# Kernel optimization log

Measured on AMD Instinct MI355X. Metric: run time of the kernel, lower is better.

The kernel has to match this reference:

```python
import jax, jax.numpy as jnp
import numpy as np

D = 768
H = 12
DK = D // H
FF = 3072
EPS = 1e-5


def layernorm(x, g, b):
    mu = jnp.mean(x, axis=-1, keepdims=True)
    var = jnp.mean((x - mu) ** 2, axis=-1, keepdims=True)
    return (x - mu) * jax.lax.rsqrt(var + EPS) * g + b


def setup_inputs() -> dict:
    key = jax.random.key(0)
    ks = jax.random.split(key, 12)
    B, S = 4, 2048
    s = 0.02
    return {
        "embedding": jax.random.normal(ks[0], (B, S, D), jnp.float32),
        "mask": jnp.ones((B, 1, 1, S), jnp.int32),
        "Wq": jax.random.normal(ks[1], (D, D), jnp.float32) * s,
        "bq": jnp.zeros((D,), jnp.float32),
        "Wk": jax.random.normal(ks[2], (D, D), jnp.float32) * s,
        "bk": jnp.zeros((D,), jnp.float32),
        "Wv": jax.random.normal(ks[3], (D, D), jnp.float32) * s,
        "bv": jnp.zeros((D,), jnp.float32),
        "Wo": jax.random.normal(ks[4], (D, D), jnp.float32) * s,
        "bo": jnp.zeros((D,), jnp.float32),
        "W1": jax.random.normal(ks[5], (D, FF), jnp.float32) * s,
        "b1": jnp.zeros((FF,), jnp.float32),
        "W2": jax.random.normal(ks[6], (FF, D), jnp.float32) * s,
        "b2": jnp.zeros((D,), jnp.float32),
        "ln_g": jnp.ones((D,), jnp.float32),
        "ln_b": jnp.zeros((D,), jnp.float32),
    }


def reference(embedding, mask, Wq, bq, Wk, bk, Wv, bv, Wo, bo, W1, b1, W2, b2, ln_g, ln_b):
    B, S, _ = embedding.shape
    # QKV projections -> [B, H, S, DK]
    def split_heads(t):
        return t.reshape(B, S, H, DK).transpose(0, 2, 1, 3)
    q = split_heads(embedding @ Wq + bq)
    k = split_heads(embedding @ Wk + bk)
    v = split_heads(embedding @ Wv + bv)
    scores = jnp.einsum("bhqd,bhkd->bhqk", q, k) / jnp.sqrt(jnp.float32(DK))
    scores = jnp.where(mask == 0, jnp.float32(-1e9), scores)
    weights = jax.nn.softmax(scores, axis=-1)  # dropout = identity (eval)
    context = jnp.einsum("bhqk,bhkd->bhqd", weights, v)
    context = context.transpose(0, 2, 1, 3).reshape(B, S, D)
    attn_out = context @ Wo + bo
    x = layernorm(attn_out + embedding, ln_g, ln_b)
    ff = jax.nn.relu(x @ W1 + b1) @ W2 + b2
    return layernorm(x + ff, ln_g, ln_b)
```

## Files before the change

kernel.cpp:

```cpp
#include <hip/hip_runtime.h>

#define D_MODEL 768
#define NHEADS  12
#define SEQ     2048
#define BATCH   4
#define FF_DIM  3072
#define NTOK    (BATCH * SEQ)

typedef short short8 __attribute__((ext_vector_type(8)));
typedef float f32x4 __attribute__((ext_vector_type(4)));
typedef float f32x16 __attribute__((ext_vector_type(16)));
typedef int int4v __attribute__((ext_vector_type(4)));
typedef int int2v __attribute__((ext_vector_type(2)));
typedef unsigned short ushort4v __attribute__((ext_vector_type(4)));
typedef float float4v __attribute__((ext_vector_type(4)));

__device__ __forceinline__ short f2bf(float x) {
  unsigned u = __builtin_bit_cast(unsigned, x);
  u += 0x7fffu + ((u >> 16) & 1u);
  return (short)(u >> 16);
}
__device__ __forceinline__ float bf2f(short x) {
  return __builtin_bit_cast(float, ((unsigned)(unsigned short)x) << 16);
}
__device__ __forceinline__ int cvtpk(float a, float b) {
  int r;
  asm("v_cvt_pk_bf16_f32 %0, %1, %2" : "=v"(r) : "v"(a), "v"(b));
  return r;
}
__device__ __forceinline__ float fexp2(float x) {
#if __has_builtin(__builtin_amdgcn_exp2f)
  return __builtin_amdgcn_exp2f(x);
#else
  return exp2f(x);
#endif
}
__device__ __forceinline__ float frcp(float x) {
#if __has_builtin(__builtin_amdgcn_rcpf)
  return __builtin_amdgcn_rcpf(x);
#else
  return 1.f / x;
#endif
}
__device__ __forceinline__ void gll16(const void* g, void* l) {
  __builtin_amdgcn_global_load_lds(
      (const __attribute__((address_space(1))) void*)g,
      (__attribute__((address_space(3))) void*)l, 16, 0, 0);
}

__device__ __forceinline__ void wt_tile(float (*T)[65], const float* __restrict__ W,
                                        short* __restrict__ Wt, int K, int N,
                                        int bx, int by, int t) {
  const int c = t & 63, rb = t >> 6;
  const int k0 = by * 64, n0 = bx * 64;
#pragma unroll
  for (int i = 0; i < 16; ++i) {
    const int r = rb * 16 + i;
    T[c][r] = W[(size_t)(k0 + r) * N + n0 + c];
  }
  __syncthreads();
#pragma unroll
  for (int j = 0; j < 16; ++j) {
    const int idx = t + j * 256;
    const int nl = idx >> 6, kl = idx & 63;
    Wt[(size_t)(n0 + nl) * K + k0 + kl] = f2bf(T[nl][kl]);
  }
}

__global__ __launch_bounds__(256) void prep(
    const float* __restrict__ Wq, const float* __restrict__ Wk, const float* __restrict__ Wv,
    const float* __restrict__ Wo, const float* __restrict__ W1, const float* __restrict__ W2,
    const float* __restrict__ bq, const float* __restrict__ bk, const float* __restrict__ bv,
    const float* __restrict__ emb,
    short* __restrict__ wqkvt, short* __restrict__ wot, short* __restrict__ w1t,
    short* __restrict__ w2t, float* __restrict__ bqkv, short* __restrict__ x0) {
  __shared__ float T[64][65];
  const int bi = blockIdx.x;
  const int t = threadIdx.x;
  if (bi < 432) {
    const int s = bi / 144, l = bi % 144;
    const float* W = (s == 0) ? Wq : (s == 1) ? Wk : Wv;
    wt_tile(T, W, wqkvt + (size_t)s * 768 * 768, 768, 768, l % 12, l / 12, t);
  } else if (bi < 576) {
    const int l = bi - 432;
    wt_tile(T, Wo, wot, 768, 768, l % 12, l / 12, t);
  } else if (bi < 1152) {
    const int l = bi - 576;
    wt_tile(T, W1, w1t, 768, 3072, l % 48, l / 48, t);
  } else if (bi < 1728) {
    const int l = bi - 1152;
    wt_tile(T, W2, w2t, 3072, 768, l % 12, l / 12, t);
  } else if (bi == 1728) {
#pragma unroll
    for (int j = 0; j < 9; ++j) {
      const int i = t + j * 256;
      bqkv[i] = (i < 768) ? bq[i] : (i < 1536) ? bk[i - 768] : bv[i - 1536];
    }
  } else {
    const int i = (bi - 1729) * 256 + t;
    float4v v = *(const float4v*)(emb + (size_t)i * 4);
    ushort4v p;
    p[0] = (unsigned short)f2bf(v[0]);
    p[1] = (unsigned short)f2bf(v[1]);
    p[2] = (unsigned short)f2bf(v[2]);
    p[3] = (unsigned short)f2bf(v[3]);
    *(ushort4v*)(x0 + (size_t)i * 4) = p;
  }
}

enum { EPI_QKV = 0, EPI_WO = 1, EPI_RELU = 2, EPI_FF = 3 };

template <int EPI>
__global__ __launch_bounds__(256) void gemm_bt(const short* __restrict__ A,
                                               const short* __restrict__ Bt,
                                               const float* __restrict__ bias,
                                               const float* __restrict__ extraF,
                                               const short* __restrict__ extraB,
                                               void* __restrict__ outp,
                                               int M, int N, int K) {
  __shared__ short As[128 * 64];
  __shared__ short Bs[128 * 64];
  const int tid = threadIdx.x;
  const int lane = tid & 63, wid = tid >> 6;
  const int wr = wid >> 1, wc = wid & 1;
  const int l16 = lane & 15, lg = lane >> 4;
  const int brow = blockIdx.y * 128, bcol = blockIdx.x * 128;

  f32x4 acc[4][4];
#pragma unroll
  for (int i = 0; i < 4; ++i)
#pragma unroll
    for (int j = 0; j < 4; ++j) acc[i][j] = (f32x4){0.f, 0.f, 0.f, 0.f};

  for (int kt = 0; kt < K; kt += 64) {
    __syncthreads();
#pragma unroll
    for (int i = 0; i < 4; ++i) {
      const int c = wid * 256 + i * 64 + lane;
      const int row = c >> 3;
      const int gc = (c & 7) ^ (row & 7);
      gll16(A + (size_t)(brow + row) * K + kt + gc * 8,
            (char*)As + (wid * 256 + i * 64) * 16);
      gll16(Bt + (size_t)(bcol + row) * K + kt + gc * 8,
            (char*)Bs + (wid * 256 + i * 64) * 16);
    }
    __syncthreads();
#pragma unroll
    for (int kc = 0; kc < 2; ++kc) {
      short8 af[4], bfr[4];
#pragma unroll
      for (int m = 0; m < 4; ++m) {
        const int row = wr * 64 + m * 16 + l16;
        const int ch = (kc * 4 + lg) ^ (row & 7);
        af[m] = *(const short8*)((const char*)As + row * 128 + ch * 16);
      }
#pragma unroll
      for (int n = 0; n < 4; ++n) {
        const int row = wc * 64 + n * 16 + l16;
        const int ch = (kc * 4 + lg) ^ (row & 7);
        bfr[n] = *(const short8*)((const char*)Bs + row * 128 + ch * 16);
      }
#pragma unroll
      for (int m = 0; m < 4; ++m)
#pragma unroll
        for (int n = 0; n < 4; ++n)
          acc[m][n] = __builtin_amdgcn_mfma_f32_16x16x32_bf16(af[m], bfr[n],
                                                              acc[m][n], 0, 0, 0);
    }
  }

  const int mbase = brow + wr * 64;
  const int nbase = bcol + wc * 64;

  if constexpr (EPI == EPI_QKV) {
    short* qb_ = (short*)outp;
    short* kb_ = qb_ + (size_t)NTOK * D_MODEL;
    short* vt_ = kb_ + (size_t)NTOK * D_MODEL;
    const int type = nbase / 768;
#pragma unroll
    for (int ni = 0; ni < 4; ++ni) {
      const int n = nbase + ni * 16 + l16;
      const float bv = bias[n];
      const int ncol = n - type * 768;
      const int h = ncol >> 6, dk = ncol & 63;
      if (type == 2) {
#pragma unroll
        for (int mi = 0; mi < 4; ++mi) {
          const int m0 = mbase + mi * 16 + lg * 4;
          const int bidx = m0 >> 11, s0 = m0 & 2047;
          ushort4v pk;
#pragma unroll
          for (int r = 0; r < 4; ++r) pk[r] = (unsigned short)f2bf(acc[mi][ni][r] + bv);
          *(ushort4v*)(vt_ + (((size_t)bidx * NHEADS + h) * 64 + dk) * SEQ + s0) = pk;
        }
      } else {
        short* o = (type == 0) ? qb_ : kb_;
        const float sc = (type == 0) ? 0.125f * 1.44269504f : 1.f;
#pragma unroll
        for (int mi = 0; mi < 4; ++mi) {
#pragma unroll
          for (int r = 0; r < 4; ++r) {
            const int m = mbase + mi * 16 + lg * 4 + r;
            const int bidx = m >> 11, sidx = m & 2047;
            o[(((size_t)bidx * NHEADS + h) * SEQ + sidx) * 64 + dk] =
                f2bf((acc[mi][ni][r] + bv) * sc);
          }
        }
      }
    }
  } else if constexpr (EPI == EPI_WO) {
    short* o = (short*)outp;
#pragma unroll
    for (int ni = 0; ni < 4; ++ni) {
      const int n = nbase + ni * 16 + l16;
      const float bv = bias[n];
#pragma unroll
      for (int mi = 0; mi < 4; ++mi)
#pragma unroll
        for (int r = 0; r < 4; ++r) {
          const int m = mbase + mi * 16 + lg * 4 + r;
          const size_t idx = (size_t)m * N + n;
          o[idx] = f2bf(acc[mi][ni][r] + bv + extraF[idx]);
        }
    }
  } else if constexpr (EPI == EPI_FF) {
    short* o = (short*)outp;
#pragma unroll
    for (int ni = 0; ni < 4; ++ni) {
      const int n = nbase + ni * 16 + l16;
      const float bv = bias[n];
#pragma unroll
      for (int mi = 0; mi < 4; ++mi)
#pragma unroll
        for (int r = 0; r < 4; ++r) {
          const int m = mbase + mi * 16 + lg * 4 + r;
          const size_t idx = (size_t)m * N + n;
          o[idx] = f2bf(acc[mi][ni][r] + bv + bf2f(extraB[idx]));
        }
    }
  } else {
    short* o = (short*)outp;
#pragma unroll
    for (int ni = 0; ni < 4; ++ni) {
      const int n = nbase + ni * 16 + l16;
      const float bv = bias[n];
#pragma unroll
      for (int mi = 0; mi < 4; ++mi)
#pragma unroll
        for (int r = 0; r < 4; ++r) {
          const int m = mbase + mi * 16 + lg * 4 + r;
          o[(size_t)m * N + n] = f2bf(fmaxf(acc[mi][ni][r] + bv, 0.f));
        }
    }
  }
}

__global__ __launch_bounds__(256) void attn_fa6(
    const short* __restrict__ Q,
    const short* __restrict__ Kb,
    const short* __restrict__ Vt,
    const int* __restrict__ mask,
    float* __restrict__ opart,
    float* __restrict__ lpart) {
  __shared__ short KsA[64 * 64], KsB[64 * 64];
  __shared__ short VsA[64 * 64], VsB[64 * 64];
  const int tid = threadIdx.x;
  const int lane = tid & 63, w = tid >> 6;
  const int l31 = lane & 31, hi = lane >> 5;

  const int i = blockIdx.x;
  const int r8 = i & 7, qq = i >> 3;
  const int bhz = ((qq >> 3) << 3) + r8;
  const int qblk = qq & 7;
  const int half = bhz / 48, bh = bhz % 48;
  const int b = bh / NHEADS;
  const int q0 = qblk * 256 + w * 64;
  const int kvbase = half * (SEQ / 2);

  const short* qpA = Q + ((size_t)bh * SEQ + q0 + l31) * 64;
  const short* qpB = qpA + 32 * 64;
  short8 qfA[4], qfB[4];
#pragma unroll
  for (int s = 0; s < 4; ++s) {
    qfA[s] = *(const short8*)(qpA + s * 16 + hi * 8);
    qfB[s] = *(const short8*)(qpB + s * 16 + hi * 8);
  }

  f32x16 o0a, o1a, o0b, o1b;
#pragma unroll
  for (int k = 0; k < 16; ++k) { o0a[k] = 0.f; o1a[k] = 0.f; o0b[k] = 0.f; o1b[k] = 0.f; }
  float lA = 0.f, lB = 0.f;

  auto stage = [&](short* Ksd, short* Vsd, int kv0) {
#pragma unroll
    for (int i2 = 0; i2 < 2; ++i2) {
      const int c = i2 * 256 + tid;
      const int row = c >> 3;
      const int gc = (c & 7) ^ (row & 7);
      gll16(Kb + ((size_t)bh * SEQ + kv0 + row) * 64 + gc * 8,
            (char*)Ksd + (i2 * 256 + w * 64) * 16);
      gll16(Vt + ((size_t)bh * 64 + row) * SEQ + kv0 + gc * 8,
            (char*)Vsd + (i2 * 256 + w * 64) * 16);
    }
  };

  stage(KsA, VsA, kvbase);
  __syncthreads();

  for (int t = 0; t < SEQ / 2 / 64; ++t) {
    const short* Ksc = (t & 1) ? KsB : KsA;
    const short* Vsc = (t & 1) ? VsB : VsA;

    const int mv = mask[(size_t)b * SEQ + kvbase + t * 64 + lane];
    const bool anym = __any(mv == 0);
    float ra = 0.f, rb_ = 0.f;
    short8 paA[4], paB[4];

#pragma unroll
    for (int ph = 0; ph < 2; ++ph) {
      f32x16 sa, sb;
#pragma unroll
      for (int k = 0; k < 16; ++k) { sa[k] = 0.f; sb[k] = 0.f; }
      const char* kr = (const char*)Ksc + (ph * 32 + l31) * 128;
#pragma unroll
      for (int slot = 0; slot < 4; ++slot) {
        const int ch = (slot * 2 + hi) ^ (l31 & 7);
        short8 kf = *(const short8*)(kr + ch * 16);
        sa = __builtin_amdgcn_mfma_f32_32x32x16_bf16(kf, qfA[slot], sa, 0, 0, 0);
        sb = __builtin_amdgcn_mfma_f32_32x32x16_bf16(kf, qfB[slot], sb, 0, 0, 0);
      }
      if (ph == 1 && t + 1 < SEQ / 2 / 64)
        stage((t & 1) ? KsA : KsB, (t & 1) ? VsA : VsB, kvbase + (t + 1) * 64);
      if (anym) {
#pragma unroll
        for (int r = 0; r < 16; ++r) {
          const int cr = ph * 32 + (r & 3) + 8 * (r >> 2) + 4 * hi;
          if (__shfl(mv, cr) == 0) { sa[r] = -1e9f; sb[r] = -1e9f; }
        }
      }
#pragma unroll
      for (int r = 0; r < 16; ++r) {
        sa[r] = fexp2(sa[r]);
        sb[r] = fexp2(sb[r]);
        ra += sa[r];
        rb_ += sb[r];
      }
#pragma unroll
      for (int ks = 0; ks < 2; ++ks) {
        const int rb0 = ks * 8;
#pragma unroll
        for (int g = 0; g < 2; ++g) {
          const f32x16& sc = g ? sb : sa;
          int x0_ = cvtpk(sc[rb0 + 0], sc[rb0 + 1]);
          int y0_ = cvtpk(sc[rb0 + 4], sc[rb0 + 5]);
          int x1_ = cvtpk(sc[rb0 + 2], sc[rb0 + 3]);
          int y1_ = cvtpk(sc[rb0 + 6], sc[rb0 + 7]);
          int4v pw;
#if __has_builtin(__builtin_amdgcn_permlane32_swap)
          int2v r0 = __builtin_amdgcn_permlane32_swap(x0_, y0_, false, false);
          int2v r1 = __builtin_amdgcn_permlane32_swap(x1_, y1_, false, false);
          pw[0] = r0[0]; pw[1] = r1[0]; pw[2] = r0[1]; pw[3] = r1[1];
#else
          const int ys0 = __shfl_xor(y0_, 32);
          const int xs0 = __shfl_xor(x0_, 32);
          const int ys1 = __shfl_xor(y1_, 32);
          const int xs1 = __shfl_xor(x1_, 32);
          pw[0] = hi ? ys0 : x0_;
          pw[1] = hi ? ys1 : x1_;
          pw[2] = hi ? y0_ : xs0;
          pw[3] = hi ? y1_ : xs1;
#endif
          const short8 pa = __builtin_bit_cast(short8, pw);
          if (g) paB[ph * 2 + ks] = pa; else paA[ph * 2 + ks] = pa;
        }
      }
    }
    lA += ra + __shfl_xor(ra, 32);
    lB += rb_ + __shfl_xor(rb_, 32);

#pragma unroll
    for (int vs = 0; vs < 4; ++vs) {
      const int vch = (vs * 2 + hi) ^ (l31 & 7);
      short8 vb0 = *(const short8*)((const char*)Vsc + l31 * 128 + vch * 16);
      short8 vb1 = *(const short8*)((const char*)Vsc + (32 + l31) * 128 + vch * 16);
      o0a = __builtin_amdgcn_mfma_f32_32x32x16_bf16(paA[vs], vb0, o0a, 0, 0, 0);
      o0b = __builtin_amdgcn_mfma_f32_32x32x16_bf16(paB[vs], vb0, o0b, 0, 0, 0);
      o1a = __builtin_amdgcn_mfma_f32_32x32x16_bf16(paA[vs], vb1, o1a, 0, 0, 0);
      o1b = __builtin_amdgcn_mfma_f32_32x32x16_bf16(paB[vs], vb1, o1b, 0, 0, 0);
    }
    __syncthreads();
  }

  float* opA = opart + ((size_t)half * BATCH * NHEADS + bh) * SEQ * 64;
#pragma unroll
  for (int r = 0; r < 16; ++r) {
    const int q = (r & 3) + 8 * (r >> 2) + 4 * hi;
    float* pa_ = opA + (size_t)(q0 + q) * 64;
    pa_[l31] = o0a[r];
    pa_[32 + l31] = o1a[r];
    float* pb_ = opA + (size_t)(q0 + 32 + q) * 64;
    pb_[l31] = o0b[r];
    pb_[32 + l31] = o1b[r];
  }
  if (lane < 32) {
    float* lp = lpart + (size_t)half * BATCH * NHEADS * SEQ + (size_t)bh * SEQ + q0;
    lp[l31] = lA;
    lp[32 + l31] = lB;
  }
}

__global__ __launch_bounds__(256) void attn_combine(const float* __restrict__ op,
                                                    const float* __restrict__ lp,
                                                    short* __restrict__ ctx) {
  const size_t HS = (size_t)BATCH * NHEADS * SEQ * 64;
  const int i4 = blockIdx.x * 256 + threadIdx.x;
  const size_t base = (size_t)i4 * 4;
  float4v a = *(const float4v*)(op + base);
  float4v c = *(const float4v*)(op + HS + base);
  const int row = (int)(base >> 6);
  const float inv = frcp(lp[row] + lp[BATCH * NHEADS * SEQ + row]);
  const int bh = row >> 11, q = row & 2047;
  const int b = bh / NHEADS, h = bh - b * NHEADS;
  const int dk = (int)(base & 63);
  ushort4v o;
#pragma unroll
  for (int j = 0; j < 4; ++j) o[j] = (unsigned short)f2bf((a[j] + c[j]) * inv);
  *(ushort4v*)(ctx + ((size_t)b * SEQ + q) * D_MODEL + h * 64 + dk) = o;
}

template <int OUT_F32>
__global__ __launch_bounds__(256) void ln_w(const short* __restrict__ y,
                                            const float* __restrict__ gw,
                                            const float* __restrict__ bw,
                                            float* __restrict__ of,
                                            short* __restrict__ ob) {
  const int lane = threadIdx.x & 63, w = threadIdx.x >> 6;
  const int row = blockIdx.x * 4 + w;
  const short* yr = y + (size_t)row * D_MODEL;
  short8 v8 = *(const short8*)(yr + lane * 8);
  ushort4v v4 = *(const ushort4v*)(yr + 512 + lane * 4);
  float f[12];
#pragma unroll
  for (int j = 0; j < 8; ++j) f[j] = bf2f(v8[j]);
#pragma unroll
  for (int j = 0; j < 4; ++j) f[8 + j] = bf2f((short)v4[j]);
  float s = 0.f, q = 0.f;
#pragma unroll
  for (int j = 0; j < 12; ++j) { s += f[j]; q += f[j] * f[j]; }
#pragma unroll
  for (int mm = 1; mm < 64; mm <<= 1) {
    s += __shfl_xor(s, mm);
    q += __shfl_xor(q, mm);
  }
  const float mu = s * (1.f / D_MODEL);
  const float rs = rsqrtf(q * (1.f / D_MODEL) - mu * mu + 1e-5f);
  float4v g0 = *(const float4v*)(gw + lane * 8);
  float4v g1 = *(const float4v*)(gw + lane * 8 + 4);
  float4v g2 = *(const float4v*)(gw + 512 + lane * 4);
  float4v b0 = *(const float4v*)(bw + lane * 8);
  float4v b1 = *(const float4v*)(bw + lane * 8 + 4);
  float4v b2 = *(const float4v*)(bw + 512 + lane * 4);
  float o[12];
#pragma unroll
  for (int j = 0; j < 4; ++j) o[j] = (f[j] - mu) * rs * g0[j] + b0[j];
#pragma unroll
  for (int j = 0; j < 4; ++j) o[4 + j] = (f[4 + j] - mu) * rs * g1[j] + b1[j];
#pragma unroll
  for (int j = 0; j < 4; ++j) o[8 + j] = (f[8 + j] - mu) * rs * g2[j] + b2[j];
  if constexpr (OUT_F32) {
    float* orow = of + (size_t)row * D_MODEL;
    float4v t0, t1, t2;
#pragma unroll
    for (int j = 0; j < 4; ++j) { t0[j] = o[j]; t1[j] = o[4 + j]; t2[j] = o[8 + j]; }
    *(float4v*)(orow + lane * 8) = t0;
    *(float4v*)(orow + lane * 8 + 4) = t1;
    *(float4v*)(orow + 512 + lane * 4) = t2;
  } else {
    short* orow = ob + (size_t)row * D_MODEL;
    ushort4v t0, t1, t2;
#pragma unroll
    for (int j = 0; j < 4; ++j) {
      t0[j] = (unsigned short)f2bf(o[j]);
      t1[j] = (unsigned short)f2bf(o[4 + j]);
      t2[j] = (unsigned short)f2bf(o[8 + j]);
    }
    *(ushort4v*)(orow + lane * 8) = t0;
    *(ushort4v*)(orow + lane * 8 + 4) = t1;
    *(ushort4v*)(orow + 512 + lane * 4) = t2;
  }
}

extern "C" void kernel_launch(void* const* d_in, const int* in_sizes, int n_in,
                              void* d_out, int out_size, void* d_ws, size_t ws_size,
                              hipStream_t stream) {
  const float* emb = (const float*)d_in[0];
  const int* mask = (const int*)d_in[1];
  const float* Wq = (const float*)d_in[2];
  const float* bq = (const float*)d_in[3];
  const float* Wk = (const float*)d_in[4];
  const float* bk = (const float*)d_in[5];
  const float* Wv = (const float*)d_in[6];
  const float* bv = (const float*)d_in[7];
  const float* Wo = (const float*)d_in[8];
  const float* bo = (const float*)d_in[9];
  const float* W1 = (const float*)d_in[10];
  const float* b1 = (const float*)d_in[11];
  const float* W2 = (const float*)d_in[12];
  const float* b2 = (const float*)d_in[13];
  const float* lng = (const float*)d_in[14];
  const float* lnb = (const float*)d_in[15];

  char* ws = (char*)d_ws;
  size_t off = 0;
  auto alloc = [&](size_t bytes) -> char* {
    char* p = ws + off;
    off = (off + bytes + 255) & ~(size_t)255;
    return p;
  };
  const size_t DD = (size_t)D_MODEL * D_MODEL;
  const size_t DF = (size_t)D_MODEL * FF_DIM;
  const size_t TD = (size_t)NTOK * D_MODEL;
  const size_t TF = (size_t)NTOK * FF_DIM;

  short* wqkvt = (short*)alloc(3 * DD * 2);
  short* wot = (short*)alloc(DD * 2);
  short* w1t = (short*)alloc(DF * 2);
  short* w2t = (short*)alloc(DF * 2);
  float* bqkv = (float*)alloc(2304 * 4);
  short* x0 = (short*)alloc(TD * 2);
  short* qkv = (short*)alloc(3 * TD * 2);
  short* aresb = (short*)alloc(TD * 2);
  short* xbf = (short*)alloc(TD * 2);
  short* hbf = (short*)alloc(TF * 2);
  short* ffresb = (short*)alloc(TD * 2);
  float* lpart = (float*)alloc(2 * (size_t)BATCH * NHEADS * SEQ * 4);
  short* qb = qkv;
  short* kb = qkv + TD;
  short* vtb = qkv + 2 * TD;
  short* ctx = x0;
  float* opart = (float*)hbf;

  prep<<<dim3(1729 + (int)(TD / 1024)), 256, 0, stream>>>(
      Wq, Wk, Wv, Wo, W1, W2, bq, bk, bv, emb, wqkvt, wot, w1t, w2t, bqkv, x0);
  gemm_bt<EPI_QKV><<<dim3(18, 64), 256, 0, stream>>>(
      x0, wqkvt, bqkv, nullptr, nullptr, qkv, NTOK, 3 * D_MODEL, D_MODEL);
  attn_fa6<<<dim3(768), 256, 0, stream>>>(qb, kb, vtb, mask, opart, lpart);
  attn_combine<<<dim3((int)((size_t)BATCH * NHEADS * SEQ * 64 / 4 / 256)), 256, 0, stream>>>(
      opart, lpart, ctx);
  gemm_bt<EPI_WO><<<dim3(6, 64), 256, 0, stream>>>(
      ctx, wot, bo, emb, nullptr, aresb, NTOK, D_MODEL, D_MODEL);
  ln_w<0><<<dim3(NTOK / 4), 256, 0, stream>>>(aresb, lng, lnb, nullptr, xbf);
  gemm_bt<EPI_RELU><<<dim3(24, 64), 256, 0, stream>>>(
      xbf, w1t, b1, nullptr, nullptr, hbf, NTOK, FF_DIM, D_MODEL);
  gemm_bt<EPI_FF><<<dim3(6, 64), 256, 0, stream>>>(
      hbf, w2t, b2, nullptr, xbf, ffresb, NTOK, D_MODEL, FF_DIM);
  ln_w<1><<<dim3(NTOK / 4), 256, 0, stream>>>(ffresb, lng, lnb, (float*)d_out, nullptr);
}
```

Before: 299.0 us.

## Store K/V in MFMA fragment layout and stream attention operands from global

The QKV GEMM epilogue now writes K and V pre-permuted into the exact per-lane fragment order the 32x32x16 MFMA operands need. The attention kernel can then load K and V straight from global memory into registers, with no LDS staging and no per-tile __syncthreads. K tiles are double-buffered in registers, and the kernel processes 32 keys per step instead of 64. This removes LDS traffic, swizzle arithmetic and block barriers, but each of the four waves now fetches the same K/V data on its own, so more load pressure falls on the caches. The last prefetch also reads one tile past each key range.

```diff
diff --git a/kernel.cpp b/kernel.cpp
--- a/kernel.cpp
+++ b/kernel.cpp
@@ -174,8 +174,8 @@
 
   if constexpr (EPI == EPI_QKV) {
     short* qb_ = (short*)outp;
-    short* kb_ = qb_ + (size_t)NTOK * D_MODEL;
-    short* vt_ = kb_ + (size_t)NTOK * D_MODEL;
+    short* kf_ = qb_ + (size_t)NTOK * D_MODEL;
+    short* vf_ = kf_ + (size_t)NTOK * D_MODEL;
     const int type = nbase / 768;
 #pragma unroll
     for (int ni = 0; ni < 4; ++ni) {
@@ -183,28 +183,45 @@
       const float bv = bias[n];
       const int ncol = n - type * 768;
       const int h = ncol >> 6, dk = ncol & 63;
-      if (type == 2) {
+      if (type == 0) {
+#pragma unroll
+        for (int mi = 0; mi < 4; ++mi) {
+#pragma unroll
+          for (int r = 0; r < 4; ++r) {
+            const int m = mbase + mi * 16 + lg * 4 + r;
+            const int bidx = m >> 11, sidx = m & 2047;
+            qb_[(((size_t)bidx * NHEADS + h) * SEQ + sidx) * 64 + dk] =
+                f2bf((acc[mi][ni][r] + bv) * (0.125f * 1.44269504f));
+          }
+        }
+      } else if (type == 1) {
+        const int slot = dk >> 4, dhi = (dk >> 3) & 1, e = dk & 7;
+#pragma unroll
+        for (int mi = 0; mi < 4; ++mi) {
+#pragma unroll
+          for (int r = 0; r < 4; ++r) {
+            const int m = mbase + mi * 16 + lg * 4 + r;
+            const int bidx = m >> 11, sidx = m & 2047;
+            const size_t bh = (size_t)bidx * NHEADS + h;
+            const size_t idx =
+                (((bh * 64 + (sidx >> 5)) * 4 + slot) * 64 + ((sidx & 31) + dhi * 32)) * 8 + e;
+            kf_[idx] = f2bf(acc[mi][ni][r] + bv);
+          }
+        }
+      } else {
+        const int dblk = dk >> 5, lanef = dk & 31;
 #pragma unroll
         for (int mi = 0; mi < 4; ++mi) {
           const int m0 = mbase + mi * 16 + lg * 4;
           const int bidx = m0 >> 11, s0 = m0 & 2047;
+          const size_t bh = (size_t)bidx * NHEADS + h;
           ushort4v pk;
 #pragma unroll
           for (int r = 0; r < 4; ++r) pk[r] = (unsigned short)f2bf(acc[mi][ni][r] + bv);
-          *(ushort4v*)(vt_ + (((size_t)bidx * NHEADS + h) * 64 + dk) * SEQ + s0) = pk;
-        }
-      } else {
-        short* o = (type == 0) ? qb_ : kb_;
-        const float sc = (type == 0) ? 0.125f * 1.44269504f : 1.f;
-#pragma unroll
-        for (int mi = 0; mi < 4; ++mi) {
-#pragma unroll
-          for (int r = 0; r < 4; ++r) {
-            const int m = mbase + mi * 16 + lg * 4 + r;
-            const int bidx = m >> 11, sidx = m & 2047;
-            o[(((size_t)bidx * NHEADS + h) * SEQ + sidx) * 64 + dk] =
-                f2bf((acc[mi][ni][r] + bv) * sc);
-          }
+          const size_t idx =
+              (((bh * 128 + (s0 >> 4)) * 2 + dblk) * 64 + (lanef + ((s0 >> 3) & 1) * 32)) * 8 +
+              (s0 & 7);
+          *(ushort4v*)(vf_ + idx) = pk;
         }
       }
     }
@@ -255,15 +272,13 @@
   }
 }
 
-__global__ __launch_bounds__(256) void attn_fa6(
+__global__ __launch_bounds__(256) void attn_fa7(
     const short* __restrict__ Q,
-    const short* __restrict__ Kb,
-    const short* __restrict__ Vt,
+    const short* __restrict__ Kf,
+    const short* __restrict__ Vf,
     const int* __restrict__ mask,
     float* __restrict__ opart,
     float* __restrict__ lpart) {
-  __shared__ short KsA[64 * 64], KsB[64 * 64];
-  __shared__ short VsA[64 * 64], VsB[64 * 64];
   const int tid = threadIdx.x;
   const int lane = tid & 63, w = tid >> 6;
   const int l31 = lane & 31, hi = lane >> 5;
@@ -275,7 +290,7 @@
   const int half = bhz / 48, bh = bhz % 48;
   const int b = bh / NHEADS;
   const int q0 = qblk * 256 + w * 64;
-  const int kvbase = half * (SEQ / 2);
+  const int kvt0 = half * 32;
 
   const short* qpA = Q + ((size_t)bh * SEQ + q0 + l31) * 64;
   const short* qpB = qpA + 32 * 64;
@@ -286,110 +301,102 @@
     qfB[s] = *(const short8*)(qpB + s * 16 + hi * 8);
   }
 
+  const short* kfb = Kf + (((size_t)bh * 64 + kvt0) * 4 * 64 + lane) * 8;
+  const short* vfb = Vf + (((size_t)bh * 128 + kvt0 * 2) * 2 * 64 + lane) * 8;
+  const int* mrow = mask + (size_t)b * SEQ + kvt0 * 32;
+
   f32x16 o0a, o1a, o0b, o1b;
 #pragma unroll
   for (int k = 0; k < 16; ++k) { o0a[k] = 0.f; o1a[k] = 0.f; o0b[k] = 0.f; o1b[k] = 0.f; }
-  float lA = 0.f, lB = 0.f;
-
-  auto stage = [&](short* Ksd, short* Vsd, int kv0) {
-#pragma unroll
-    for (int i2 = 0; i2 < 2; ++i2) {
-      const int c = i2 * 256 + tid;
-      const int row = c >> 3;
-      const int gc = (c & 7) ^ (row & 7);
-      gll16(Kb + ((size_t)bh * SEQ + kv0 + row) * 64 + gc * 8,
-            (char*)Ksd + (i2 * 256 + w * 64) * 16);
-      gll16(Vt + ((size_t)bh * 64 + row) * SEQ + kv0 + gc * 8,
-            (char*)Vsd + (i2 * 256 + w * 64) * 16);
+  float raA = 0.f, raB = 0.f;
+
+  short8 kfX[4], kfY[4];
+#pragma unroll
+  for (int s = 0; s < 4; ++s) kfX[s] = *(const short8*)(kfb + (size_t)s * 512);
+
+  auto body = [&](int t, short8* kcur, short8* knext) {
+    short8 vf[4];
+#pragma unroll
+    for (int j = 0; j < 4; ++j)
+      vf[j] = *(const short8*)(vfb + ((size_t)t * 4 + j) * 512);
+
+    f32x16 sa, sb;
+#pragma unroll
+    for (int k = 0; k < 16; ++k) { sa[k] = 0.f; sb[k] = 0.f; }
+#pragma unroll
+    for (int s = 0; s < 4; ++s) {
+      sa = __builtin_amdgcn_mfma_f32_32x32x16_bf16(kcur[s], qfA[s], sa, 0, 0, 0);
+      sb = __builtin_amdgcn_mfma_f32_32x32x16_bf16(kcur[s], qfB[s], sb, 0, 0, 0);
+    }
+
+#pragma unroll
+    for (int s = 0; s < 4; ++s)
+      knext[s] = *(const short8*)(kfb + ((size_t)(t + 1) * 4 + s) * 512);
+
+    const int mv = mrow[t * 32 + l31];
+    if (__any(mv == 0)) {
+#pragma unroll
+      for (int r = 0; r < 16; ++r) {
+        const int cr = (r & 3) + 8 * (r >> 2) + 4 * hi;
+        if (__shfl(mv, cr) == 0) { sa[r] = -1e9f; sb[r] = -1e9f; }
+      }
+    }
+
+#pragma unroll
+    for (int r = 0; r < 16; ++r) {
+      sa[r] = fexp2(sa[r]);
+      sb[r] = fexp2(sb[r]);
+      raA += sa[r];
+      raB += sb[r];
+    }
+
+    short8 paA[2], paB[2];
+#pragma unroll
+    for (int ks = 0; ks < 2; ++ks) {
+      const int rb0 = ks * 8;
+#pragma unroll
+      for (int g = 0; g < 2; ++g) {
+        const f32x16& sc = g ? sb : sa;
+        int x0_ = cvtpk(sc[rb0 + 0], sc[rb0 + 1]);
+        int y0_ = cvtpk(sc[rb0 + 4], sc[rb0 + 5]);
+        int x1_ = cvtpk(sc[rb0 + 2], sc[rb0 + 3]);
+        int y1_ = cvtpk(sc[rb0 + 6], sc[rb0 + 7]);
+        int4v pw;
+#if __has_builtin(__builtin_amdgcn_permlane32_swap)
+        int2v r0 = __builtin_amdgcn_permlane32_swap(x0_, y0_, false, false);
+        int2v r1 = __builtin_amdgcn_permlane32_swap(x1_, y1_, false, false);
+        pw[0] = r0[0]; pw[1] = r1[0]; pw[2] = r0[1]; pw[3] = r1[1];
+#else
+        const int ys0 = __shfl_xor(y0_, 32);
+        const int xs0 = __shfl_xor(x0_, 32);
+        const int ys1 = __shfl_xor(y1_, 32);
+        const int xs1 = __shfl_xor(x1_, 32);
+        pw[0] = hi ? ys0 : x0_;
+        pw[1] = hi ? ys1 : x1_;
+        pw[2] = hi ? y0_ : xs0;
+        pw[3] = hi ? y1_ : xs1;
+#endif
+        const short8 pa = __builtin_bit_cast(short8, pw);
+        if (g) paB[ks] = pa; else paA[ks] = pa;
+      }
+    }
+
+#pragma unroll
+    for (int ks = 0; ks < 2; ++ks) {
+      o0a = __builtin_amdgcn_mfma_f32_32x32x16_bf16(paA[ks], vf[ks * 2 + 0], o0a, 0, 0, 0);
+      o0b = __builtin_amdgcn_mfma_f32_32x32x16_bf16(paB[ks], vf[ks * 2 + 0], o0b, 0, 0, 0);
+      o1a = __builtin_amdgcn_mfma_f32_32x32x16_bf16(paA[ks], vf[ks * 2 + 1], o1a, 0, 0, 0);
+      o1b = __builtin_amdgcn_mfma_f32_32x32x16_bf16(paB[ks], vf[ks * 2 + 1], o1b, 0, 0, 0);
     }
   };
 
-  stage(KsA, VsA, kvbase);
-  __syncthreads();
-
-  for (int t = 0; t < SEQ / 2 / 64; ++t) {
-    const short* Ksc = (t & 1) ? KsB : KsA;
-    const short* Vsc = (t & 1) ? VsB : VsA;
-
-    const int mv = mask[(size_t)b * SEQ + kvbase + t * 64 + lane];
-    const bool anym = __any(mv == 0);
-    float ra = 0.f, rb_ = 0.f;
-    short8 paA[4], paB[4];
-
-#pragma unroll
-    for (int ph = 0; ph < 2; ++ph) {
-      f32x16 sa, sb;
-#pragma unroll
-      for (int k = 0; k < 16; ++k) { sa[k] = 0.f; sb[k] = 0.f; }
-      const char* kr = (const char*)Ksc + (ph * 32 + l31) * 128;
-#pragma unroll
-      for (int slot = 0; slot < 4; ++slot) {
-        const int ch = (slot * 2 + hi) ^ (l31 & 7);
-        short8 kf = *(const short8*)(kr + ch * 16);
-        sa = __builtin_amdgcn_mfma_f32_32x32x16_bf16(kf, qfA[slot], sa, 0, 0, 0);
-        sb = __builtin_amdgcn_mfma_f32_32x32x16_bf16(kf, qfB[slot], sb, 0, 0, 0);
-      }
-      if (ph == 1 && t + 1 < SEQ / 2 / 64)
-        stage((t & 1) ? KsA : KsB, (t & 1) ? VsA : VsB, kvbase + (t + 1) * 64);
-      if (anym) {
-#pragma unroll
-        for (int r = 0; r < 16; ++r) {
-          const int cr = ph * 32 + (r & 3) + 8 * (r >> 2) + 4 * hi;
-          if (__shfl(mv, cr) == 0) { sa[r] = -1e9f; sb[r] = -1e9f; }
-        }
-      }
-#pragma unroll
-      for (int r = 0; r < 16; ++r) {
-        sa[r] = fexp2(sa[r]);
-        sb[r] = fexp2(sb[r]);
-        ra += sa[r];
-        rb_ += sb[r];
-      }
-#pragma unroll
-      for (int ks = 0; ks < 2; ++ks) {
-        const int rb0 = ks * 8;
-#pragma unroll
-        for (int g = 0; g < 2; ++g) {
-          const f32x16& sc = g ? sb : sa;
-          int x0_ = cvtpk(sc[rb0 + 0], sc[rb0 + 1]);
-          int y0_ = cvtpk(sc[rb0 + 4], sc[rb0 + 5]);
-          int x1_ = cvtpk(sc[rb0 + 2], sc[rb0 + 3]);
-          int y1_ = cvtpk(sc[rb0 + 6], sc[rb0 + 7]);
-          int4v pw;
-#if __has_builtin(__builtin_amdgcn_permlane32_swap)
-          int2v r0 = __builtin_amdgcn_permlane32_swap(x0_, y0_, false, false);
-          int2v r1 = __builtin_amdgcn_permlane32_swap(x1_, y1_, false, false);
-          pw[0] = r0[0]; pw[1] = r1[0]; pw[2] = r0[1]; pw[3] = r1[1];
-#else
-          const int ys0 = __shfl_xor(y0_, 32);
-          const int xs0 = __shfl_xor(x0_, 32);
-          const int ys1 = __shfl_xor(y1_, 32);
-          const int xs1 = __shfl_xor(x1_, 32);
-          pw[0] = hi ? ys0 : x0_;
-          pw[1] = hi ? ys1 : x1_;
-          pw[2] = hi ? y0_ : xs0;
-          pw[3] = hi ? y1_ : xs1;
-#endif
-          const short8 pa = __builtin_bit_cast(short8, pw);
-          if (g) paB[ph * 2 + ks] = pa; else paA[ph * 2 + ks] = pa;
-        }
-      }
-    }
-    lA += ra + __shfl_xor(ra, 32);
-    lB += rb_ + __shfl_xor(rb_, 32);
-
-#pragma unroll
-    for (int vs = 0; vs < 4; ++vs) {
-      const int vch = (vs * 2 + hi) ^ (l31 & 7);
-      short8 vb0 = *(const short8*)((const char*)Vsc + l31 * 128 + vch * 16);
-      short8 vb1 = *(const short8*)((const char*)Vsc + (32 + l31) * 128 + vch * 16);
-      o0a = __builtin_amdgcn_mfma_f32_32x32x16_bf16(paA[vs], vb0, o0a, 0, 0, 0);
-      o0b = __builtin_amdgcn_mfma_f32_32x32x16_bf16(paB[vs], vb0, o0b, 0, 0, 0);
-      o1a = __builtin_amdgcn_mfma_f32_32x32x16_bf16(paA[vs], vb1, o1a, 0, 0, 0);
-      o1b = __builtin_amdgcn_mfma_f32_32x32x16_bf16(paB[vs], vb1, o1b, 0, 0, 0);
-    }
-    __syncthreads();
-  }
+  for (int tt = 0; tt < 16; ++tt) {
+    body(2 * tt, kfX, kfY);
+    body(2 * tt + 1, kfY, kfX);
+  }
+
+  const float lA = raA + __shfl_xor(raA, 32);
+  const float lB = raB + __shfl_xor(raB, 32);
 
   float* opA = opart + ((size_t)half * BATCH * NHEADS + bh) * SEQ * 64;
 #pragma unroll
@@ -535,8 +542,8 @@
   short* ffresb = (short*)alloc(TD * 2);
   float* lpart = (float*)alloc(2 * (size_t)BATCH * NHEADS * SEQ * 4);
   short* qb = qkv;
-  short* kb = qkv + TD;
-  short* vtb = qkv + 2 * TD;
+  short* kfr = qkv + TD;
+  short* vfr = qkv + 2 * TD;
   short* ctx = x0;
   float* opart = (float*)hbf;
 
@@ -544,7 +551,7 @@
       Wq, Wk, Wv, Wo, W1, W2, bq, bk, bv, emb, wqkvt, wot, w1t, w2t, bqkv, x0);
   gemm_bt<EPI_QKV><<<dim3(18, 64), 256, 0, stream>>>(
       x0, wqkvt, bqkv, nullptr, nullptr, qkv, NTOK, 3 * D_MODEL, D_MODEL);
-  attn_fa6<<<dim3(768), 256, 0, stream>>>(qb, kb, vtb, mask, opart, lpart);
+  attn_fa7<<<dim3(768), 256, 0, stream>>>(qb, kfr, vfr, mask, opart, lpart);
   attn_combine<<<dim3((int)((size_t)BATCH * NHEADS * SEQ * 64 / 4 / 256)), 256, 0, stream>>>(
       opart, lpart, ctx);
   gemm_bt<EPI_WO><<<dim3(6, 64), 256, 0, stream>>>(
```

New measurement: 312.5 us. +4.5%, slower.

## Store attention partials in bf16, raise MFMA wave priority, defer row-sum shuffles

Applied to the files above, without the earlier changes.

The split-KV attention kernel now writes its partial output accumulators as bf16 instead of fp32, which halves the write and re-read traffic between attention and the combine kernel. The combine kernel processes 8 elements per thread and launches half as many blocks. The MFMA sections are wrapped in s_setprio to favour matrix issue, the first QK MFMA starts from a zero constant instead of re-zeroing accumulators, and the cross-half row-sum shuffle moves out of the loop to the end. Rounding the unnormalised partials to bf16 adds a small precision loss.

```diff
diff --git a/kernel.cpp b/kernel.cpp
--- a/kernel.cpp
+++ b/kernel.cpp
@@ -260,7 +260,7 @@
     const short* __restrict__ Kb,
     const short* __restrict__ Vt,
     const int* __restrict__ mask,
-    float* __restrict__ opart,
+    short* __restrict__ opart,
     float* __restrict__ lpart) {
   __shared__ short KsA[64 * 64], KsB[64 * 64];
   __shared__ short VsA[64 * 64], VsB[64 * 64];
@@ -286,6 +286,10 @@
     qfB[s] = *(const short8*)(qpB + s * 16 + hi * 8);
   }
 
+  f32x16 kZero;
+#pragma unroll
+  for (int k = 0; k < 16; ++k) kZero[k] = 0.f;
+
   f32x16 o0a, o1a, o0b, o1b;
 #pragma unroll
   for (int k = 0; k < 16; ++k) { o0a[k] = 0.f; o1a[k] = 0.f; o0b[k] = 0.f; o1b[k] = 0.f; }
@@ -313,22 +317,27 @@
 
     const int mv = mask[(size_t)b * SEQ + kvbase + t * 64 + lane];
     const bool anym = __any(mv == 0);
-    float ra = 0.f, rb_ = 0.f;
     short8 paA[4], paB[4];
 
 #pragma unroll
     for (int ph = 0; ph < 2; ++ph) {
       f32x16 sa, sb;
-#pragma unroll
-      for (int k = 0; k < 16; ++k) { sa[k] = 0.f; sb[k] = 0.f; }
       const char* kr = (const char*)Ksc + (ph * 32 + l31) * 128;
-#pragma unroll
-      for (int slot = 0; slot < 4; ++slot) {
+      __builtin_amdgcn_s_setprio(1);
+      {
+        const int ch = hi ^ (l31 & 7);
+        short8 kf = *(const short8*)(kr + ch * 16);
+        sa = __builtin_amdgcn_mfma_f32_32x32x16_bf16(kf, qfA[0], kZero, 0, 0, 0);
+        sb = __builtin_amdgcn_mfma_f32_32x32x16_bf16(kf, qfB[0], kZero, 0, 0, 0);
+      }
+#pragma unroll
+      for (int slot = 1; slot < 4; ++slot) {
         const int ch = (slot * 2 + hi) ^ (l31 & 7);
         short8 kf = *(const short8*)(kr + ch * 16);
         sa = __builtin_amdgcn_mfma_f32_32x32x16_bf16(kf, qfA[slot], sa, 0, 0, 0);
         sb = __builtin_amdgcn_mfma_f32_32x32x16_bf16(kf, qfB[slot], sb, 0, 0, 0);
       }
+      __builtin_amdgcn_s_setprio(0);
       if (ph == 1 && t + 1 < SEQ / 2 / 64)
         stage((t & 1) ? KsA : KsB, (t & 1) ? VsA : VsB, kvbase + (t + 1) * 64);
       if (anym) {
@@ -342,8 +351,8 @@
       for (int r = 0; r < 16; ++r) {
         sa[r] = fexp2(sa[r]);
         sb[r] = fexp2(sb[r]);
-        ra += sa[r];
-        rb_ += sb[r];
+        lA += sa[r];
+        lB += sb[r];
       }
 #pragma unroll
       for (int ks = 0; ks < 2; ++ks) {
@@ -375,9 +384,8 @@
         }
       }
     }
-    lA += ra + __shfl_xor(ra, 32);
-    lB += rb_ + __shfl_xor(rb_, 32);
-
+
+    __builtin_amdgcn_s_setprio(1);
 #pragma unroll
     for (int vs = 0; vs < 4; ++vs) {
       const int vch = (vs * 2 + hi) ^ (l31 & 7);
@@ -388,19 +396,23 @@
       o1a = __builtin_amdgcn_mfma_f32_32x32x16_bf16(paA[vs], vb1, o1a, 0, 0, 0);
       o1b = __builtin_amdgcn_mfma_f32_32x32x16_bf16(paB[vs], vb1, o1b, 0, 0, 0);
     }
+    __builtin_amdgcn_s_setprio(0);
     __syncthreads();
   }
 
-  float* opA = opart + ((size_t)half * BATCH * NHEADS + bh) * SEQ * 64;
+  lA += __shfl_xor(lA, 32);
+  lB += __shfl_xor(lB, 32);
+
+  short* opA = opart + ((size_t)half * BATCH * NHEADS + bh) * SEQ * 64;
 #pragma unroll
   for (int r = 0; r < 16; ++r) {
     const int q = (r & 3) + 8 * (r >> 2) + 4 * hi;
-    float* pa_ = opA + (size_t)(q0 + q) * 64;
-    pa_[l31] = o0a[r];
-    pa_[32 + l31] = o1a[r];
-    float* pb_ = opA + (size_t)(q0 + 32 + q) * 64;
-    pb_[l31] = o0b[r];
-    pb_[32 + l31] = o1b[r];
+    short* pa_ = opA + (size_t)(q0 + q) * 64;
+    pa_[l31] = f2bf(o0a[r]);
+    pa_[32 + l31] = f2bf(o1a[r]);
+    short* pb_ = opA + (size_t)(q0 + 32 + q) * 64;
+    pb_[l31] = f2bf(o0b[r]);
+    pb_[32 + l31] = f2bf(o1b[r]);
   }
   if (lane < 32) {
     float* lp = lpart + (size_t)half * BATCH * NHEADS * SEQ + (size_t)bh * SEQ + q0;
@@ -409,23 +421,23 @@
   }
 }
 
-__global__ __launch_bounds__(256) void attn_combine(const float* __restrict__ op,
+__global__ __launch_bounds__(256) void attn_combine(const short* __restrict__ op,
                                                     const float* __restrict__ lp,
                                                     short* __restrict__ ctx) {
   const size_t HS = (size_t)BATCH * NHEADS * SEQ * 64;
-  const int i4 = blockIdx.x * 256 + threadIdx.x;
-  const size_t base = (size_t)i4 * 4;
-  float4v a = *(const float4v*)(op + base);
-  float4v c = *(const float4v*)(op + HS + base);
+  const int i8 = blockIdx.x * 256 + threadIdx.x;
+  const size_t base = (size_t)i8 * 8;
+  short8 a = *(const short8*)(op + base);
+  short8 c = *(const short8*)(op + HS + base);
   const int row = (int)(base >> 6);
   const float inv = frcp(lp[row] + lp[BATCH * NHEADS * SEQ + row]);
   const int bh = row >> 11, q = row & 2047;
   const int b = bh / NHEADS, h = bh - b * NHEADS;
   const int dk = (int)(base & 63);
-  ushort4v o;
-#pragma unroll
-  for (int j = 0; j < 4; ++j) o[j] = (unsigned short)f2bf((a[j] + c[j]) * inv);
-  *(ushort4v*)(ctx + ((size_t)b * SEQ + q) * D_MODEL + h * 64 + dk) = o;
+  short8 o;
+#pragma unroll
+  for (int j = 0; j < 8; ++j) o[j] = f2bf((bf2f(a[j]) + bf2f(c[j])) * inv);
+  *(short8*)(ctx + ((size_t)b * SEQ + q) * D_MODEL + h * 64 + dk) = o;
 }
 
 template <int OUT_F32>
@@ -538,14 +550,14 @@
   short* kb = qkv + TD;
   short* vtb = qkv + 2 * TD;
   short* ctx = x0;
-  float* opart = (float*)hbf;
+  short* opart = hbf;
 
   prep<<<dim3(1729 + (int)(TD / 1024)), 256, 0, stream>>>(
       Wq, Wk, Wv, Wo, W1, W2, bq, bk, bv, emb, wqkvt, wot, w1t, w2t, bqkv, x0);
   gemm_bt<EPI_QKV><<<dim3(18, 64), 256, 0, stream>>>(
       x0, wqkvt, bqkv, nullptr, nullptr, qkv, NTOK, 3 * D_MODEL, D_MODEL);
   attn_fa6<<<dim3(768), 256, 0, stream>>>(qb, kb, vtb, mask, opart, lpart);
-  attn_combine<<<dim3((int)((size_t)BATCH * NHEADS * SEQ * 64 / 4 / 256)), 256, 0, stream>>>(
+  attn_combine<<<dim3((int)((size_t)BATCH * NHEADS * SEQ * 64 / 8 / 256)), 256, 0, stream>>>(
       opart, lpart, ctx);
   gemm_bt<EPI_WO><<<dim3(6, 64), 256, 0, stream>>>(
       ctx, wot, bo, emb, nullptr, aresb, NTOK, D_MODEL, D_MODEL);
```

Measured after the change: 283.6 us. 1.05x faster.
